# Kernel optimization log

Measured on AMD Instinct MI355X. Metric: run time of the kernel, lower is better.

Reference implementation:

```python
import jax, jax.numpy as jnp
import numpy as np

MGC_SIZE = 80
COND_DIM = 256
LSTM_SIZE = 500
UP_SCALE = 64  # prod([4,4,4])
TEMPERATURE = 1.0
EPS_MIN = -7.0


def setup_inputs() -> dict:
    key = jax.random.key(0)
    ks = jax.random.split(key, 10)
    B, T_FRAMES = 16, 32
    T = T_FRAMES * UP_SCALE  # 2048 decode steps
    s = 0.02  # weight scale for numerical stability (logvar goes through exp)
    return {
        "mgc": jax.random.normal(ks[0], (B, T_FRAMES, MGC_SIZE), dtype=jnp.float32),
        "eps": jax.random.normal(ks[1], (B, T), dtype=jnp.float32),
        # UpsampleNet stand-in: linear projection mgc_size->256, then repeat x64 in time
        "W_up": jax.random.normal(ks[2], (MGC_SIZE, COND_DIM), dtype=jnp.float32) * s,
        "b_up": jnp.zeros((COND_DIM,), dtype=jnp.float32),
        # LSTM (PyTorch layout, gate order i,f,g,o)
        "W_ih": jax.random.normal(ks[3], (4 * LSTM_SIZE, COND_DIM + 1), dtype=jnp.float32) * s,
        "W_hh": jax.random.normal(ks[4], (4 * LSTM_SIZE, LSTM_SIZE), dtype=jnp.float32) * s,
        "b_ih": jax.random.normal(ks[5], (4 * LSTM_SIZE,), dtype=jnp.float32) * s,
        "b_hh": jax.random.normal(ks[6], (4 * LSTM_SIZE,), dtype=jnp.float32) * s,
        # output Linear(lstm_size, 2)
        "W_out": jax.random.normal(ks[7], (2, LSTM_SIZE), dtype=jnp.float32) * s,
        "b_out": jnp.zeros((2,), dtype=jnp.float32),
    }


def reference(mgc, eps, W_up, b_up, W_ih, W_hh, b_ih, b_hh, W_out, b_out):
    B = mgc.shape[0]
    # conditioning: (B, T_frames, 80) -> (B, T, 256)
    cond = jnp.repeat(mgc @ W_up + b_up, UP_SCALE, axis=1)
    bias = b_ih + b_hh

    def step(carry, xs):
        h, c, x_prev = carry              # (B,H), (B,H), (B,)
        cond_t, eps_t = xs                # (B,256), (B,)
        inp = jnp.concatenate([cond_t, x_prev[:, None]], axis=1)  # (B,257)
        gates = inp @ W_ih.T + h @ W_hh.T + bias                  # (B,4H)
        i, f, g, o = jnp.split(gates, 4, axis=1)
        i = jax.nn.sigmoid(i)
        f = jax.nn.sigmoid(f)
        g = jnp.tanh(g)
        o = jax.nn.sigmoid(o)
        c = f * c + i * g
        h = o * jnp.tanh(c)
        out = h @ W_out.T + b_out         # (B,2)
        mean = jnp.tanh(out[:, 0])
        logvar = jnp.maximum(out[:, 1], EPS_MIN)  # clamp(min=eps_min)
        zz = mean + (eps_t * TEMPERATURE) * jnp.exp(logvar)
        return (h, c, zz), (mean, logvar, zz)

    h0 = jnp.zeros((B, LSTM_SIZE), dtype=mgc.dtype)
    c0 = jnp.zeros((B, LSTM_SIZE), dtype=mgc.dtype)
    x0 = jnp.zeros((B,), dtype=mgc.dtype)
    xs = (cond.transpose(1, 0, 2), eps.T)  # time-major
    _, (mean, logvar, zz) = jax.lax.scan(step, (h0, c0, x0), xs)
    # back to (B, T)
    return mean.T, logvar.T, zz.T
```

## Files before the change

kernel.cpp:

```cpp
#include <hip/hip_runtime.h>
#include <stdint.h>

#define TSTEPS 2048
#define NB     16
#define HDIM   500
#define NSLICE 16
#define NTHR   256
#define NBLK   256
#define GSTR   20
#define HSTR   264

#define HBASE(P) ((size_t)(P) * 4096)
#define PBASE(P) (8192 + (size_t)(P) * 256)
#define DONE64   8704

typedef __attribute__((ext_vector_type(8))) short s16x8;
typedef __attribute__((ext_vector_type(4))) float f32x4;

__device__ __forceinline__ unsigned short f2bf(float f) {
    unsigned u = __float_as_uint(f);
    u += 0x7FFFu + ((u >> 16) & 1u);
    return (unsigned short)(u >> 16);
}
__device__ __forceinline__ float bf2f(uint32_t hw) { return __uint_as_float(hw << 16); }
__device__ __forceinline__ float sigm(float x)   { return __fdividef(1.f, 1.f + __expf(-x)); }
__device__ __forceinline__ float tanhf_(float x) { return 1.f - __fdividef(2.f, __expf(2.f * x) + 1.f); }

__global__ void zero_ws_kernel(uint32_t* p, int n) {
    int i = blockIdx.x * blockDim.x + threadIdx.x;
    if (i < n) p[i] = 0u;
}

__global__ __launch_bounds__(NTHR, 1) void wavernn_persist(
    const float* __restrict__ mgc,  const float* __restrict__ eps,
    const float* __restrict__ Wup,  const float* __restrict__ bup,
    const float* __restrict__ Wih,  const float* __restrict__ Whh,
    const float* __restrict__ bih,  const float* __restrict__ bhh,
    const float* __restrict__ Wout, const float* __restrict__ bout,
    float* __restrict__ out, uint64_t* __restrict__ hb)
{
    if (blockIdx.x >= NSLICE) {
        const uint64_t* done = hb + DONE64;
        float a = (float)threadIdx.x * 1e-3f + (float)blockIdx.x;
        while (__hip_atomic_load(done, __ATOMIC_RELAXED,
                                 __HIP_MEMORY_SCOPE_AGENT) == 0ull) {
            #pragma unroll 16
            for (int i = 0; i < 4096; ++i) a = __builtin_fmaf(a, 1.0000001f, 1e-7f);
        }
        asm volatile("" :: "v"(a));
        return;
    }

    const int s    = blockIdx.x;
    const int tid  = threadIdx.x;
    const int lane = tid & 63;
    const int wave = tid >> 6;
    const int l16  = lane & 15;
    const int g    = lane >> 4;

    __shared__ __align__(16) uint32_t h_l[16 * HSTR];
    __shared__ __align__(16) float gates_l[NB * 132];
    __shared__ __align__(16) float gcond[128 * GSTR];
    __shared__ __align__(16) float condT[256 * NB];
    __shared__ __align__(16) float mgcl[NB * 80];
    __shared__ __align__(16) float eps_l[128 * NB];
    __shared__ __align__(16) float zz_l[NB];

    s16x8 bfr[2][16];
    float wihl[2];
    #pragma unroll
    for (int t2 = 0; t2 < 2; ++t2) {
        const int q    = t2 * 16 + l16;
        const int hidx = s * 32 + q;
        const bool valid = hidx < HDIM;
        const int grow = wave * HDIM + hidx;
        wihl[t2] = valid ? Wih[grow * 257 + 256] : 0.f;
        #pragma unroll
        for (int kk = 0; kk < 16; ++kk) {
            const int k0 = kk * 32 + g * 8;
            s16x8 r;
            #pragma unroll
            for (int j = 0; j < 8; ++j) {
                const int k = k0 + j;
                const float v = (valid && k < HDIM) ? Whh[grow * HDIM + k] : 0.f;
                r[j] = (short)f2bf(v);
            }
            bfr[t2][kk] = r;
        }
    }
    const int b_e = tid >> 4;
    const int qh  = tid & 15;
    const int q0  = 2 * qh, q1 = q0 + 1;
    const int k0g = s * 32 + q0, k1g = s * 32 + q1;
    const float w0q0 = (k0g < HDIM) ? Wout[k0g]        : 0.f;
    const float w0q1 = (k1g < HDIM) ? Wout[k1g]        : 0.f;
    const float w1q0 = (k0g < HDIM) ? Wout[HDIM + k0g] : 0.f;
    const float w1q1 = (k1g < HDIM) ? Wout[HDIM + k1g] : 0.f;
    const float bout0 = bout[0], bout1 = bout[1];
    float cst0 = 0.f, cst1 = 0.f;

    auto rebuild = [&](int f) {
        for (int i = tid; i < NB * 80; i += NTHR) {
            const int b = i / 80, m = i - b * 80;
            mgcl[i] = mgc[(b * 32 + f) * 80 + m];
        }
        for (int i = tid; i < 64 * NB; i += NTHR) {
            const int st = i >> 4, b = i & 15;
            eps_l[((f & 1) * 64 + st) * NB + b] = eps[b * 2048 + f * 64 + st];
        }
        __syncthreads();
        {
            const int c = tid;
            float a[NB];
            #pragma unroll
            for (int b = 0; b < NB; ++b) a[b] = bup[c];
            for (int m = 0; m < 80; ++m) {
                const float w = Wup[m * 256 + c];
                #pragma unroll
                for (int b = 0; b < NB; ++b) a[b] += mgcl[b * 80 + m] * w;
            }
            #pragma unroll
            for (int b = 0; b < NB; ++b) condT[c * NB + b] = a[b];
        }
        __syncthreads();
        {
            const int n = tid >> 1, kc = tid & 1;
            const int gate = n >> 5, q = n & 31;
            const int hidx = s * 32 + q;
            const bool valid = hidx < HDIM;
            const int grow = gate * HDIM + hidx;
            float a[NB];
            #pragma unroll
            for (int b = 0; b < NB; ++b) a[b] = 0.f;
            if (valid) {
                const float* wr = Wih + (size_t)grow * 257 + kc * 128;
                for (int k = 0; k < 128; ++k) {
                    const float w = wr[k];
                    const float* cp = &condT[(kc * 128 + k) * NB];
                    #pragma unroll
                    for (int b = 0; b < NB; ++b) a[b] += cp[b] * w;
                }
            }
            if (kc == 0) {
                const float bias = valid ? (bih[grow] + bhh[grow]) : 0.f;
                #pragma unroll
                for (int b = 0; b < NB; ++b) gcond[n * GSTR + b] = a[b] + bias;
            }
            __syncthreads();
            if (kc == 1) {
                #pragma unroll
                for (int b = 0; b < NB; ++b) gcond[n * GSTR + b] += a[b];
            }
        }
        __syncthreads();
    };

    for (int i = tid; i < 16 * HSTR; i += NTHR) h_l[i] = 0u;
    rebuild(0);

    const int gp = tid >> 4, gb = tid & 15;

    for (int t = 0; t < TSTEPS; ++t) {
        if (t > 0) {
            const uint32_t* src = (const uint32_t*)(hb + HBASE((t & 1) ^ 1)
                                                    + (size_t)gp * 256 + gb * 16);
            const uint32_t want = (uint32_t)t;
            uint4 u[8];
            int guard = 0;
            while (true) {
                #pragma unroll
                for (int i = 0; i < 8; ++i)
                    asm volatile("global_load_dwordx4 %0, %1, off sc0 sc1"
                                 : "=v"(u[i]) : "v"(src + i * 4));
                asm volatile("s_waitcnt vmcnt(0)" ::: "memory");
                __builtin_amdgcn_sched_barrier(0);
                bool ok = true;
                #pragma unroll
                for (int i = 0; i < 8; ++i)
                    ok &= (u[i].y == want) & (u[i].w == want);
                if (ok || ++guard > (1 << 18)) break;
            }
            #pragma unroll
            for (int q = 0; q < 4; ++q) {
                uint4 w;
                w.x = u[2 * q].x;     w.y = u[2 * q].z;
                w.z = u[2 * q + 1].x; w.w = u[2 * q + 1].z;
                *(uint4*)&h_l[gp * HSTR + (q * 16 + gb) * 4] = w;
            }
        }
        __syncthreads();

        uint64_t pv[4];
        if (t > 0) {
            const uint64_t* pb = hb + PBASE((t & 1) ^ 1);
            #pragma unroll
            for (int j = 0; j < 4; ++j)
                pv[j] = __hip_atomic_load(pb + l16 * 16 + (g + 4 * j),
                                          __ATOMIC_RELAXED, __HIP_MEMORY_SCOPE_AGENT);
        }

        const int n0 = wave * 32 + l16;
        f32x4 acc0a = *(const f32x4*)&gcond[n0 * GSTR + g * 4];
        f32x4 acc1a = *(const f32x4*)&gcond[(n0 + 16) * GSTR + g * 4];
        f32x4 acc0b = {0.f, 0.f, 0.f, 0.f};
        f32x4 acc1b = {0.f, 0.f, 0.f, 0.f};
        s16x8 hfr[16];
        #pragma unroll
        for (int p = 0; p < 16; ++p)
            hfr[p] = *(const s16x8*)&h_l[p * HSTR + lane * 4];
        #pragma unroll
        for (int kk = 0; kk < 8; ++kk) {
            acc0a = __builtin_amdgcn_mfma_f32_16x16x32_bf16(hfr[kk],     bfr[0][kk],     acc0a, 0, 0, 0);
            acc1a = __builtin_amdgcn_mfma_f32_16x16x32_bf16(hfr[kk],     bfr[1][kk],     acc1a, 0, 0, 0);
            acc0b = __builtin_amdgcn_mfma_f32_16x16x32_bf16(hfr[kk + 8], bfr[0][kk + 8], acc0b, 0, 0, 0);
            acc1b = __builtin_amdgcn_mfma_f32_16x16x32_bf16(hfr[kk + 8], bfr[1][kk + 8], acc1b, 0, 0, 0);
        }

        if (t > 0) {
            const uint64_t* pb = hb + PBASE((t & 1) ^ 1);
            const uint32_t want = (uint32_t)t;
            int guard = 0;
            while (true) {
                bool ok = true;
                #pragma unroll
                for (int j = 0; j < 4; ++j) ok &= ((uint32_t)(pv[j] >> 32) == want);
                if (ok || ++guard > (1 << 18)) break;
                #pragma unroll
                for (int j = 0; j < 4; ++j)
                    pv[j] = __hip_atomic_load(pb + l16 * 16 + (g + 4 * j),
                                              __ATOMIC_RELAXED, __HIP_MEMORY_SCOPE_AGENT);
            }
            float o0[4], o1[4];
            #pragma unroll
            for (int j = 0; j < 4; ++j) {
                o0[j] = bf2f((uint32_t)pv[j] & 0xFFFFu);
                o1[j] = bf2f(((uint32_t)pv[j]) >> 16);
            }
            #pragma unroll
            for (int m = 1; m < 16; m <<= 1) {
                #pragma unroll
                for (int j = 0; j < 4; ++j) {
                    o0[j] += __shfl_xor(o0[j], m);
                    o1[j] += __shfl_xor(o1[j], m);
                }
            }
            const int row = (t - 1) & 127;
            float meanj[4], lvj[4], zzj[4];
            #pragma unroll
            for (int j = 0; j < 4; ++j) {
                const int B = g + 4 * j;
                meanj[j] = tanhf_(o0[j] + bout0);
                lvj[j]   = fmaxf(o1[j] + bout1, -7.f);
                zzj[j]   = meanj[j] + eps_l[row * NB + B] * __expf(lvj[j]);
            }
            if (l16 == 0) {
                #pragma unroll
                for (int j = 0; j < 4; ++j) zz_l[g + 4 * j] = zzj[j];
            }
            __builtin_amdgcn_sched_barrier(0);
            if (s == 0 && wave == 0 && l16 == 0) {
                #pragma unroll
                for (int j = 0; j < 4; ++j) {
                    const int B = g + 4 * j;
                    out[         B * 2048 + (t - 1)] = meanj[j];
                    out[32768 +  B * 2048 + (t - 1)] = lvj[j];
                    out[65536 +  B * 2048 + (t - 1)] = zzj[j];
                }
            }
        }

        f32x4 r0 = acc0a + acc0b;
        f32x4 r1 = acc1a + acc1b;
        if (t > 0) {
            const f32x4 zzq = *(const f32x4*)&zz_l[g * 4];
            r0 += zzq * wihl[0];
            r1 += zzq * wihl[1];
        }
        #pragma unroll
        for (int v = 0; v < 4; ++v) {
            gates_l[(g * 4 + v) * 132 + n0]      = r0[v];
            gates_l[(g * 4 + v) * 132 + n0 + 16] = r1[v];
        }
        __syncthreads();

        {
            const uint64_t tag = ((uint64_t)(uint32_t)(t + 1)) << 32;
            float po0, po1;
            uint32_t hp = 0;
            {
                const float gi = gates_l[b_e * 132 +      q0];
                const float gf = gates_l[b_e * 132 + 32 + q0];
                const float gg = gates_l[b_e * 132 + 64 + q0];
                const float go = gates_l[b_e * 132 + 96 + q0];
                cst0 = sigm(gf) * cst0 + sigm(gi) * tanhf_(gg);
                const float h = sigm(go) * tanhf_(cst0);
                if (k0g < HDIM) hp |= (uint32_t)f2bf(h);
                po0 = h * w0q0; po1 = h * w1q0;
            }
            {
                const float gi = gates_l[b_e * 132 +      q1];
                const float gf = gates_l[b_e * 132 + 32 + q1];
                const float gg = gates_l[b_e * 132 + 64 + q1];
                const float go = gates_l[b_e * 132 + 96 + q1];
                cst1 = sigm(gf) * cst1 + sigm(gi) * tanhf_(gg);
                const float h = sigm(go) * tanhf_(cst1);
                if (k1g < HDIM) hp |= ((uint32_t)f2bf(h)) << 16;
                po0 += h * w0q1; po1 += h * w1q1;
            }
            __hip_atomic_store(hb + HBASE(t & 1) + (size_t)s * 256 + b_e * 16 + qh,
                               (uint64_t)hp | tag,
                               __ATOMIC_RELAXED, __HIP_MEMORY_SCOPE_AGENT);
            po0 += __shfl_xor(po0, 1);  po1 += __shfl_xor(po1, 1);
            po0 += __shfl_xor(po0, 2);  po1 += __shfl_xor(po1, 2);
            po0 += __shfl_xor(po0, 4);  po1 += __shfl_xor(po1, 4);
            po0 += __shfl_xor(po0, 8);  po1 += __shfl_xor(po1, 8);
            if (qh == 0) {
                const uint32_t pk = (uint32_t)f2bf(po0) | ((uint32_t)f2bf(po1) << 16);
                __hip_atomic_store(hb + PBASE(t & 1) + s * 16 + b_e,
                                   (uint64_t)pk | tag,
                                   __ATOMIC_RELAXED, __HIP_MEMORY_SCOPE_AGENT);
            }
        }

        if (((t + 1) & 63) == 0 && (t + 1) < TSTEPS) rebuild((t + 1) >> 6);
    }

    if (s == 0 && wave == 0) {
        const uint64_t* pb = hb + PBASE(1);
        const uint32_t want = (uint32_t)TSTEPS;
        uint64_t pv[4];
        #pragma unroll
        for (int j = 0; j < 4; ++j)
            pv[j] = __hip_atomic_load(pb + l16 * 16 + (g + 4 * j),
                                      __ATOMIC_RELAXED, __HIP_MEMORY_SCOPE_AGENT);
        int guard = 0;
        while (true) {
            bool ok = true;
            #pragma unroll
            for (int j = 0; j < 4; ++j) ok &= ((uint32_t)(pv[j] >> 32) == want);
            if (ok || ++guard > (1 << 18)) break;
            #pragma unroll
            for (int j = 0; j < 4; ++j)
                pv[j] = __hip_atomic_load(pb + l16 * 16 + (g + 4 * j),
                                          __ATOMIC_RELAXED, __HIP_MEMORY_SCOPE_AGENT);
        }
        float o0[4], o1[4];
        #pragma unroll
        for (int j = 0; j < 4; ++j) {
            o0[j] = bf2f((uint32_t)pv[j] & 0xFFFFu);
            o1[j] = bf2f(((uint32_t)pv[j]) >> 16);
        }
        #pragma unroll
        for (int m = 1; m < 16; m <<= 1) {
            #pragma unroll
            for (int j = 0; j < 4; ++j) {
                o0[j] += __shfl_xor(o0[j], m);
                o1[j] += __shfl_xor(o1[j], m);
            }
        }
        if (l16 == 0) {
            #pragma unroll
            for (int j = 0; j < 4; ++j) {
                const int B = g + 4 * j;
                const float mean = tanhf_(o0[j] + bout0);
                const float lvv  = fmaxf(o1[j] + bout1, -7.f);
                const float zzv  = mean + eps_l[127 * NB + B] * __expf(lvv);
                out[         B * 2048 + 2047] = mean;
                out[32768 +  B * 2048 + 2047] = lvv;
                out[65536 +  B * 2048 + 2047] = zzv;
            }
        }
    }
    if (s == 0 && tid == 0)
        __hip_atomic_store(hb + DONE64, 1ull,
                           __ATOMIC_RELAXED, __HIP_MEMORY_SCOPE_AGENT);
}

extern "C" void kernel_launch(void* const* d_in, const int* in_sizes, int n_in,
                              void* d_out, int out_size, void* d_ws, size_t ws_size,
                              hipStream_t stream) {
    const float* mgc  = (const float*)d_in[0];
    const float* eps  = (const float*)d_in[1];
    const float* Wup  = (const float*)d_in[2];
    const float* bup  = (const float*)d_in[3];
    const float* Wih  = (const float*)d_in[4];
    const float* Whh  = (const float*)d_in[5];
    const float* bih  = (const float*)d_in[6];
    const float* bhh  = (const float*)d_in[7];
    const float* Wout = (const float*)d_in[8];
    const float* bout = (const float*)d_in[9];

    uint64_t* hb = (uint64_t*)d_ws;

    zero_ws_kernel<<<69, 256, 0, stream>>>((uint32_t*)hb, 17410);
    wavernn_persist<<<NBLK, NTHR, 0, stream>>>(mgc, eps, Wup, bup, Wih, Whh,
                                               bih, bhh, Wout, bout,
                                               (float*)d_out, hb);
}
```

Measured before the change: 9.167 ms.

## Merge output partials into hidden-state records and batch cross-block exchange

Packs the output-projection partial sums into spare bits of the per-step hidden-state records, which removes the separate partials buffer and its second spin-wait. Each block stages its records in shared memory and publishes them with wide 16-byte stores from half the threads. Consumers poll wider chunks with a short sleep, and block 0 buffers the outputs in shared memory and flushes them every 64 steps instead of writing each step. The cost is an 8-bit step tag in place of the full counter, extra shared memory, and an additional barrier per step.

Result: slower. 11.13 ms (+21.4%).

```diff
diff --git a/kernel.cpp b/kernel.cpp
--- a/kernel.cpp
+++ b/kernel.cpp
@@ -11,11 +11,11 @@
 #define HSTR   264
 
 #define HBASE(P) ((size_t)(P) * 4096)
-#define PBASE(P) (8192 + (size_t)(P) * 256)
-#define DONE64   8704
+#define DONE64   8192
 
 typedef __attribute__((ext_vector_type(8))) short s16x8;
 typedef __attribute__((ext_vector_type(4))) float f32x4;
+typedef __attribute__((ext_vector_type(4))) unsigned int u32x4;
 
 __device__ __forceinline__ unsigned short f2bf(float f) {
     unsigned u = __float_as_uint(f);
@@ -65,6 +65,11 @@
     __shared__ __align__(16) float mgcl[NB * 80];
     __shared__ __align__(16) float eps_l[128 * NB];
     __shared__ __align__(16) float zz_l[NB];
+    __shared__ __align__(16) uint64_t pub_l[256];
+    __shared__ __align__(16) uint32_t part_l[16 * 17];
+    __shared__ __align__(16) float stage_m[1024];
+    __shared__ __align__(16) float stage_v[1024];
+    __shared__ __align__(16) float stage_z[1024];
 
     s16x8 bfr[2][16];
     float wihl[2];
@@ -158,45 +163,108 @@
     for (int i = tid; i < 16 * HSTR; i += NTHR) h_l[i] = 0u;
     rebuild(0);
 
-    const int gp = tid >> 4, gb = tid & 15;
-
-    for (int t = 0; t < TSTEPS; ++t) {
+    for (int t = 0; t <= TSTEPS; ++t) {
+        if (t == TSTEPS && s != 0) break;
+
+        if (t > 0 && tid < 128) {
+            const int i = tid;
+            const int p = i >> 3;
+            const uint32_t want8 = (uint32_t)t & 0xFFu;
+            uint64_t v[32];
+            if (p == s) {
+                const int lb = 32 * (i & 7);
+                #pragma unroll
+                for (int k = 0; k < 32; ++k) v[k] = pub_l[lb + k];
+            } else {
+                u32x4 u[16];
+                const uint32_t* src = (const uint32_t*)(hb + HBASE((t & 1) ^ 1)
+                                                        + (size_t)(2 * i) * 16);
+                int guard = 0;
+                while (true) {
+                    #pragma unroll
+                    for (int k = 0; k < 16; ++k)
+                        asm volatile("global_load_dwordx4 %0, %1, off sc0 sc1"
+                                     : "=v"(u[k]) : "v"(src + k * 4));
+                    asm volatile("s_waitcnt vmcnt(0)" ::: "memory");
+                    __builtin_amdgcn_sched_barrier(0);
+                    bool ok = true;
+                    #pragma unroll
+                    for (int k = 0; k < 16; ++k)
+                        ok &= ((u[k][1] & 0xFFu) == want8) & ((u[k][3] & 0xFFu) == want8);
+                    if (ok || ++guard > (1 << 18)) break;
+                    __builtin_amdgcn_s_sleep(1);
+                }
+                #pragma unroll
+                for (int k = 0; k < 16; ++k) {
+                    v[2 * k]     = (uint64_t)u[k][0] | ((uint64_t)u[k][1] << 32);
+                    v[2 * k + 1] = (uint64_t)u[k][2] | ((uint64_t)u[k][3] << 32);
+                }
+            }
+            #pragma unroll
+            for (int rr = 0; rr < 2; ++rr) {
+                const int b = (2 * i + rr) & 15;
+                const uint64_t* rv = v + rr * 16;
+                #pragma unroll
+                for (int c = 0; c < 4; ++c) {
+                    u32x4 w;
+                    w[0] = (uint32_t)rv[4 * c];     w[1] = (uint32_t)rv[4 * c + 1];
+                    w[2] = (uint32_t)rv[4 * c + 2]; w[3] = (uint32_t)rv[4 * c + 3];
+                    *(u32x4*)&h_l[p * HSTR + (c * 16 + b) * 4] = w;
+                }
+                part_l[p * 17 + b] = (uint32_t)((rv[0] >> 40) & 0xFFFFu)
+                                   | ((uint32_t)((rv[1] >> 40) & 0xFFFFu) << 16);
+            }
+        }
+        __syncthreads();
+
         if (t > 0) {
-            const uint32_t* src = (const uint32_t*)(hb + HBASE((t & 1) ^ 1)
-                                                    + (size_t)gp * 256 + gb * 16);
-            const uint32_t want = (uint32_t)t;
-            uint4 u[8];
-            int guard = 0;
-            while (true) {
-                #pragma unroll
-                for (int i = 0; i < 8; ++i)
-                    asm volatile("global_load_dwordx4 %0, %1, off sc0 sc1"
-                                 : "=v"(u[i]) : "v"(src + i * 4));
-                asm volatile("s_waitcnt vmcnt(0)" ::: "memory");
-                __builtin_amdgcn_sched_barrier(0);
-                bool ok = true;
-                #pragma unroll
-                for (int i = 0; i < 8; ++i)
-                    ok &= (u[i].y == want) & (u[i].w == want);
-                if (ok || ++guard > (1 << 18)) break;
-            }
-            #pragma unroll
-            for (int q = 0; q < 4; ++q) {
-                uint4 w;
-                w.x = u[2 * q].x;     w.y = u[2 * q].z;
-                w.z = u[2 * q + 1].x; w.w = u[2 * q + 1].z;
-                *(uint4*)&h_l[gp * HSTR + (q * 16 + gb) * 4] = w;
-            }
-        }
-        __syncthreads();
-
-        uint64_t pv[4];
-        if (t > 0) {
-            const uint64_t* pb = hb + PBASE((t & 1) ^ 1);
-            #pragma unroll
-            for (int j = 0; j < 4; ++j)
-                pv[j] = __hip_atomic_load(pb + l16 * 16 + (g + 4 * j),
-                                          __ATOMIC_RELAXED, __HIP_MEMORY_SCOPE_AGENT);
+            float o0[4], o1[4];
+            #pragma unroll
+            for (int j = 0; j < 4; ++j) {
+                const uint32_t pp = part_l[l16 * 17 + (g * 4 + j)];
+                o0[j] = bf2f(pp & 0xFFFFu);
+                o1[j] = bf2f(pp >> 16);
+            }
+            #pragma unroll
+            for (int m = 1; m < 16; m <<= 1) {
+                #pragma unroll
+                for (int j = 0; j < 4; ++j) {
+                    o0[j] += __shfl_xor(o0[j], m);
+                    o1[j] += __shfl_xor(o1[j], m);
+                }
+            }
+            const int row = (t - 1) & 127;
+            const int r64 = (t - 1) & 63;
+            #pragma unroll
+            for (int j = 0; j < 4; ++j) {
+                const int B = g * 4 + j;
+                const float mean = tanhf_(o0[j] + bout0);
+                const float lv   = fmaxf(o1[j] + bout1, -7.f);
+                const float zzv  = mean + eps_l[row * NB + B] * __expf(lv);
+                if (l16 == 0) {
+                    zz_l[B] = zzv;
+                    if (s == 0) {
+                        stage_m[r64 * 16 + B] = mean;
+                        stage_v[r64 * 16 + B] = lv;
+                        stage_z[r64 * 16 + B] = zzv;
+                    }
+                }
+            }
+            __builtin_amdgcn_sched_barrier(0);
+        }
+
+        if (t == TSTEPS) {
+            __syncthreads();
+            for (int k = tid; k < 1024; k += NTHR) {
+                const int r = k >> 4, b = k & 15;
+                out[         b * 2048 + 31 * 64 + r] = stage_m[k];
+                out[32768 +  b * 2048 + 31 * 64 + r] = stage_v[k];
+                out[65536 +  b * 2048 + 31 * 64 + r] = stage_z[k];
+            }
+            if (tid == 0)
+                __hip_atomic_store(hb + DONE64, 1ull,
+                                   __ATOMIC_RELAXED, __HIP_MEMORY_SCOPE_AGENT);
+            break;
         }
 
         const int n0 = wave * 32 + l16;
@@ -216,59 +284,6 @@
             acc1b = __builtin_amdgcn_mfma_f32_16x16x32_bf16(hfr[kk + 8], bfr[1][kk + 8], acc1b, 0, 0, 0);
         }
 
-        if (t > 0) {
-            const uint64_t* pb = hb + PBASE((t & 1) ^ 1);
-            const uint32_t want = (uint32_t)t;
-            int guard = 0;
-            while (true) {
-                bool ok = true;
-                #pragma unroll
-                for (int j = 0; j < 4; ++j) ok &= ((uint32_t)(pv[j] >> 32) == want);
-                if (ok || ++guard > (1 << 18)) break;
-                #pragma unroll
-                for (int j = 0; j < 4; ++j)
-                    pv[j] = __hip_atomic_load(pb + l16 * 16 + (g + 4 * j),
-                                              __ATOMIC_RELAXED, __HIP_MEMORY_SCOPE_AGENT);
-            }
-            float o0[4], o1[4];
-            #pragma unroll
-            for (int j = 0; j < 4; ++j) {
-                o0[j] = bf2f((uint32_t)pv[j] & 0xFFFFu);
-                o1[j] = bf2f(((uint32_t)pv[j]) >> 16);
-            }
-            #pragma unroll
-            for (int m = 1; m < 16; m <<= 1) {
-                #pragma unroll
-                for (int j = 0; j < 4; ++j) {
-                    o0[j] += __shfl_xor(o0[j], m);
-                    o1[j] += __shfl_xor(o1[j], m);
-                }
-            }
-            const int row = (t - 1) & 127;
-            float meanj[4], lvj[4], zzj[4];
-            #pragma unroll
-            for (int j = 0; j < 4; ++j) {
-                const int B = g + 4 * j;
-                meanj[j] = tanhf_(o0[j] + bout0);
-                lvj[j]   = fmaxf(o1[j] + bout1, -7.f);
-                zzj[j]   = meanj[j] + eps_l[row * NB + B] * __expf(lvj[j]);
-            }
-            if (l16 == 0) {
-                #pragma unroll
-                for (int j = 0; j < 4; ++j) zz_l[g + 4 * j] = zzj[j];
-            }
-            __builtin_amdgcn_sched_barrier(0);
-            if (s == 0 && wave == 0 && l16 == 0) {
-                #pragma unroll
-                for (int j = 0; j < 4; ++j) {
-                    const int B = g + 4 * j;
-                    out[         B * 2048 + (t - 1)] = meanj[j];
-                    out[32768 +  B * 2048 + (t - 1)] = lvj[j];
-                    out[65536 +  B * 2048 + (t - 1)] = zzj[j];
-                }
-            }
-        }
-
         f32x4 r0 = acc0a + acc0b;
         f32x4 r1 = acc1a + acc1b;
         if (t > 0) {
@@ -284,7 +299,7 @@
         __syncthreads();
 
         {
-            const uint64_t tag = ((uint64_t)(uint32_t)(t + 1)) << 32;
+            const uint64_t tagb = ((uint64_t)(uint32_t)((t + 1) & 0xFF)) << 32;
             float po0, po1;
             uint32_t hp = 0;
             {
@@ -307,73 +322,36 @@
                 if (k1g < HDIM) hp |= ((uint32_t)f2bf(h)) << 16;
                 po0 += h * w0q1; po1 += h * w1q1;
             }
-            __hip_atomic_store(hb + HBASE(t & 1) + (size_t)s * 256 + b_e * 16 + qh,
-                               (uint64_t)hp | tag,
-                               __ATOMIC_RELAXED, __HIP_MEMORY_SCOPE_AGENT);
             po0 += __shfl_xor(po0, 1);  po1 += __shfl_xor(po1, 1);
             po0 += __shfl_xor(po0, 2);  po1 += __shfl_xor(po1, 2);
             po0 += __shfl_xor(po0, 4);  po1 += __shfl_xor(po1, 4);
             po0 += __shfl_xor(po0, 8);  po1 += __shfl_xor(po1, 8);
-            if (qh == 0) {
-                const uint32_t pk = (uint32_t)f2bf(po0) | ((uint32_t)f2bf(po1) << 16);
-                __hip_atomic_store(hb + PBASE(t & 1) + s * 16 + b_e,
-                                   (uint64_t)pk | tag,
-                                   __ATOMIC_RELAXED, __HIP_MEMORY_SCOPE_AGENT);
-            }
-        }
-
+            uint64_t rec = (uint64_t)hp | tagb;
+            if (qh == 0) rec |= ((uint64_t)f2bf(po0)) << 40;
+            if (qh == 1) rec |= ((uint64_t)f2bf(po1)) << 40;
+            pub_l[b_e * 16 + qh] = rec;
+        }
+        __syncthreads();
+
+        if (tid >= 128) {
+            const int i = tid - 128;
+            const u32x4 val = *(const u32x4*)&pub_l[2 * i];
+            const uint64_t* gdst = hb + HBASE(t & 1) + (size_t)s * 256 + 2 * i;
+            asm volatile("global_store_dwordx4 %0, %1, off sc0 sc1"
+                         :: "v"(gdst), "v"(val) : "memory");
+        }
+
+        if (s == 0 && t > 0 && (t & 63) == 0 && tid >= 128) {
+            const int fo = (t >> 6) - 1;
+            for (int k = tid - 128; k < 1024; k += 128) {
+                const int r = k >> 4, b = k & 15;
+                out[         b * 2048 + fo * 64 + r] = stage_m[k];
+                out[32768 +  b * 2048 + fo * 64 + r] = stage_v[k];
+                out[65536 +  b * 2048 + fo * 64 + r] = stage_z[k];
+            }
+        }
         if (((t + 1) & 63) == 0 && (t + 1) < TSTEPS) rebuild((t + 1) >> 6);
     }
-
-    if (s == 0 && wave == 0) {
-        const uint64_t* pb = hb + PBASE(1);
-        const uint32_t want = (uint32_t)TSTEPS;
-        uint64_t pv[4];
-        #pragma unroll
-        for (int j = 0; j < 4; ++j)
-            pv[j] = __hip_atomic_load(pb + l16 * 16 + (g + 4 * j),
-                                      __ATOMIC_RELAXED, __HIP_MEMORY_SCOPE_AGENT);
-        int guard = 0;
-        while (true) {
-            bool ok = true;
-            #pragma unroll
-            for (int j = 0; j < 4; ++j) ok &= ((uint32_t)(pv[j] >> 32) == want);
-            if (ok || ++guard > (1 << 18)) break;
-            #pragma unroll
-            for (int j = 0; j < 4; ++j)
-                pv[j] = __hip_atomic_load(pb + l16 * 16 + (g + 4 * j),
-                                          __ATOMIC_RELAXED, __HIP_MEMORY_SCOPE_AGENT);
-        }
-        float o0[4], o1[4];
-        #pragma unroll
-        for (int j = 0; j < 4; ++j) {
-            o0[j] = bf2f((uint32_t)pv[j] & 0xFFFFu);
-            o1[j] = bf2f(((uint32_t)pv[j]) >> 16);
-        }
-        #pragma unroll
-        for (int m = 1; m < 16; m <<= 1) {
-            #pragma unroll
-            for (int j = 0; j < 4; ++j) {
-                o0[j] += __shfl_xor(o0[j], m);
-                o1[j] += __shfl_xor(o1[j], m);
-            }
-        }
-        if (l16 == 0) {
-            #pragma unroll
-            for (int j = 0; j < 4; ++j) {
-                const int B = g + 4 * j;
-                const float mean = tanhf_(o0[j] + bout0);
-                const float lvv  = fmaxf(o1[j] + bout1, -7.f);
-                const float zzv  = mean + eps_l[127 * NB + B] * __expf(lvv);
-                out[         B * 2048 + 2047] = mean;
-                out[32768 +  B * 2048 + 2047] = lvv;
-                out[65536 +  B * 2048 + 2047] = zzv;
-            }
-        }
-    }
-    if (s == 0 && tid == 0)
-        __hip_atomic_store(hb + DONE64, 1ull,
-                           __ATOMIC_RELAXED, __HIP_MEMORY_SCOPE_AGENT);
 }
 
 extern "C" void kernel_launch(void* const* d_in, const int* in_sizes, int n_in,
@@ -392,7 +370,7 @@
 
     uint64_t* hb = (uint64_t*)d_ws;
 
-    zero_ws_kernel<<<69, 256, 0, stream>>>((uint32_t*)hb, 17410);
+    zero_ws_kernel<<<65, 256, 0, stream>>>((uint32_t*)hb, 16386);
     wavernn_persist<<<NBLK, NTHR, 0, stream>>>(mgc, eps, Wup, bup, Wih, Whh,
                                                bih, bhh, Wout, bout,
                                                (float*)d_out, hb);
```
